# Performance work log

Measured on AMD Instinct MI355X. Metric: run time of the kernel, lower is better.

Reference implementation:

```python
import jax, jax.numpy as jnp
import numpy as np

B, N = 2, 2048
TOP_K = 48
NUM_RBF = 16
MAX_REL = 32            # max_relative_feature
NUM_POS = 16            # num_positional_embeddings
EDGE_FEATURES = 128
EDGE_IN = NUM_POS + NUM_RBF * 25  # 416
POS_IN = 2 * MAX_REL + 2          # 66 one-hot classes


def setup_inputs() -> dict:
    key = jax.random.key(0)
    k0, k1, k2, k3 = jax.random.split(key, 4)
    X = jax.random.normal(k0, (B, N, 4, 3), dtype=jnp.float32) * 3.0
    mask = jnp.ones((B, N), dtype=jnp.float32)
    R_idx = jnp.arange(B * N, dtype=jnp.int32).reshape(B, N)
    chain_labels = jax.random.randint(k1, (B, N), 0, 4).astype(jnp.int32)
    W_pos = 0.05 * jax.random.normal(k2, (POS_IN, NUM_POS), dtype=jnp.float32)
    b_pos = jnp.zeros((NUM_POS,), dtype=jnp.float32)
    W_edge = 0.05 * jax.random.normal(k3, (EDGE_IN, EDGE_FEATURES), dtype=jnp.float32)
    b_edge = jnp.zeros((EDGE_FEATURES,), dtype=jnp.float32)
    return {"X": X, "mask": mask, "R_idx": R_idx, "chain_labels": chain_labels,
            "W_pos": W_pos, "b_pos": b_pos, "W_edge": W_edge, "b_edge": b_edge}


def _rbf(D):
    # D: [..., K] -> [..., K, NUM_RBF]
    mu = jnp.linspace(2.0, 22.0, NUM_RBF)        # D_min=2, D_max=22
    sigma = (22.0 - 2.0) / NUM_RBF               # 1.25
    return jnp.exp(-(((D[..., None] - mu) / sigma) ** 2))


def _pair_dist(A, Bc):
    # A, Bc: [B, N, 3] -> [B, N, N]
    return jnp.sqrt(jnp.sum((A[:, :, None, :] - Bc[:, None, :, :]) ** 2, axis=-1) + 1e-6)


def reference(X, mask, R_idx, chain_labels, W_pos, b_pos, W_edge, b_edge):
    # virtual Cbeta from backbone geometry
    b = X[:, :, 1, :] - X[:, :, 0, :]
    c = X[:, :, 2, :] - X[:, :, 1, :]
    a = jnp.cross(b, c, axis=-1)
    Cb = -0.58273431 * a + 0.56802827 * b - 0.54067466 * c + X[:, :, 1, :]
    Ca, Nat, Cat, Oat = X[:, :, 1, :], X[:, :, 0, :], X[:, :, 2, :], X[:, :, 3, :]

    # masked Ca-Ca distances + k nearest neighbors
    mask2 = mask[:, None, :] * mask[:, :, None]
    D = mask2 * _pair_dist(Ca, Ca)
    D_adjust = D + (1.0 - mask2) * jnp.max(D, axis=-1, keepdims=True)
    neg_D, E_idx = jax.lax.top_k(-D_adjust, min(TOP_K, N))  # smallest distances
    D_neighbors = -neg_D                                     # [B, N, K]

    rbfs = [_rbf(D_neighbors)]
    pairs = [(Nat, Nat), (Cat, Cat), (Oat, Oat), (Cb, Cb),
             (Ca, Nat), (Ca, Cat), (Ca, Oat), (Ca, Cb),
             (Nat, Cat), (Nat, Oat), (Nat, Cb), (Cb, Cat), (Cb, Oat), (Oat, Cat),
             (Nat, Ca), (Cat, Ca), (Oat, Ca), (Cb, Ca),
             (Cat, Nat), (Oat, Nat), (Cb, Nat), (Cat, Cb), (Oat, Cb), (Cat, Oat)]
    for A_, B_ in pairs:  # fixed structural set of 24 atom-pair types
        Dab = _pair_dist(A_, B_)                          # [B, N, N]
        Dn = jnp.take_along_axis(Dab, E_idx, axis=2)      # [B, N, K]
        rbfs.append(_rbf(Dn))
    RBF_all = jnp.concatenate(rbfs, axis=-1)              # [B, N, K, 25*NUM_RBF]

    # relative positional / chain features at the gathered neighbors
    offset = R_idx[:, :, None] - R_idx[:, None, :]
    offset = jnp.take_along_axis(offset, E_idx, axis=2)   # [B, N, K]
    d_chains = (chain_labels[:, :, None] == chain_labels[:, None, :]).astype(jnp.int32)
    E_chains = jnp.take_along_axis(d_chains, E_idx, axis=2)

    d = jnp.clip(offset + MAX_REL, 0, 2 * MAX_REL)
    d = d * E_chains + (1 - E_chains) * (2 * MAX_REL + 1)
    d_onehot = jax.nn.one_hot(d, POS_IN, dtype=jnp.float32)  # [B, N, K, 66]
    E_positional = d_onehot @ W_pos + b_pos                  # [B, N, K, 16]

    E = jnp.concatenate((E_positional, RBF_all), axis=-1)    # [B, N, K, 416]
    E = E @ W_edge + b_edge                                  # [B, N, K, 128]
    return E, E_idx
```

## Files before the change

### kernel.cpp

```cpp
#include <hip/hip_runtime.h>
#include <hip/hip_bf16.h>
#include <stdint.h>

#define BB   2
#define NN   2048
#define BN   (BB*NN)
#define KTOP 48
#define EIN  416
#define EF   128

typedef __attribute__((ext_vector_type(8))) short s8v;
typedef __attribute__((ext_vector_type(4))) float f32x4;
typedef __attribute__((ext_vector_type(4))) unsigned int u32x4;
typedef unsigned short u16;
typedef unsigned int u32;
typedef unsigned long long u64;

__device__ __constant__ int cPA[25] = {1,0,2,3,4,1,1,1,1,0,0,0,4,4,3,0,2,3,4,2,3,4,2,3,2};
__device__ __constant__ int cPB[25] = {1,0,2,3,4,0,2,3,4,2,3,4,2,3,2,1,1,1,1,0,0,0,4,4,3};

__device__ __forceinline__ u16 bf16u(float x) {
  __hip_bfloat16 h = __float2bfloat16(x);
  return *reinterpret_cast<u16*>(&h);
}
__device__ __forceinline__ u32 cvtpk(float lo, float hi) {
  u32 r;
  asm("v_cvt_pk_bf16_f32 %0, %1, %2" : "=v"(r) : "v"(lo), "v"(hi));
  return r;
}

__global__ __launch_bounds__(256) void prep_kernel(const float* __restrict__ X,
                                                   const float* __restrict__ W_edge,
                                                   float* __restrict__ atoms5p,
                                                   float* __restrict__ capack4,
                                                   u16* __restrict__ wtf) {
  int tid = blockIdx.x * 256 + threadIdx.x;
  if (tid < EIN * EF) {
    int k = tid >> 7, n = tid & 127;
    wtf[((size_t)(k >> 3)) * 1024 + n * 8 + (k & 7)] = bf16u(W_edge[tid]);
  } else if (tid < EIN * EF + BN) {
    int idx = tid - EIN * EF;
    const float* x = X + (size_t)idx * 12;
    float Nx = x[0], Ny = x[1], Nz = x[2];
    float Cax = x[3], Cay = x[4], Caz = x[5];
    float Cx = x[6], Cy = x[7], Cz = x[8];
    float Ox = x[9], Oy = x[10], Oz = x[11];
    float bx = Cax - Nx, by = Cay - Ny, bz = Caz - Nz;
    float cx = Cx - Cax, cy = Cy - Cay, cz = Cz - Caz;
    float ax = by * cz - bz * cy;
    float ay = bz * cx - bx * cz;
    float az = bx * cy - by * cx;
    float Cbx = -0.58273431f * ax + 0.56802827f * bx - 0.54067466f * cx + Cax;
    float Cby = -0.58273431f * ay + 0.56802827f * by - 0.54067466f * cy + Cay;
    float Cbz = -0.58273431f * az + 0.56802827f * bz - 0.54067466f * cz + Caz;
    f32x4* o = (f32x4*)(atoms5p + (size_t)idx * 20);
    o[0] = (f32x4){Nx, Ny, Nz, 0.f};
    o[1] = (f32x4){Cax, Cay, Caz, 0.f};
    o[2] = (f32x4){Cx, Cy, Cz, 0.f};
    o[3] = (f32x4){Ox, Oy, Oz, 0.f};
    o[4] = (f32x4){Cbx, Cby, Cbz, 0.f};
    *(f32x4*)(capack4 + (size_t)idx * 4) = (f32x4){Cax, Cay, Caz, 0.f};
  }
}

__device__ __forceinline__ u32 blockExclScan(u32 v, u32* scanw, int t) {
  int lane = t & 63, w = t >> 6;
  u32 inc = v;
#pragma unroll
  for (int off = 1; off < 64; off <<= 1) {
    u32 o = __shfl_up(inc, off);
    if (lane >= off) inc += o;
  }
  if (lane == 63) scanw[w] = inc;
  __syncthreads();
  u32 base = 0;
  for (int ww = 0; ww < w; ++ww) base += scanw[ww];
  __syncthreads();
  return base + inc - v;
}

template<int NB, bool CHKPREF>
__device__ __forceinline__ void radix_round(u32* hist, u32* scanw, u32* selinfo, int t,
                                            const u32* kv, u32 pref, int prefShift,
                                            int binShift, u32 binMask, u32 r) {
  const int PB = NB / 256;
#pragma unroll
  for (int q = 0; q < PB / 4; ++q)
    *(u32x4*)&hist[t * PB + q * 4] = (u32x4){0, 0, 0, 0};
  __syncthreads();
#pragma unroll
  for (int s = 0; s < 8; ++s) {
    bool ok = (!CHKPREF) || ((kv[s] >> prefShift) == pref);
    if (ok) atomicAdd(&hist[(kv[s] >> binShift) & binMask], 1u);
  }
  __syncthreads();
  u32 loc[PB];
  u32 sum = 0;
#pragma unroll
  for (int q = 0; q < PB / 4; ++q) {
    u32x4 lv = *(u32x4*)&hist[t * PB + q * 4];
    loc[q * 4 + 0] = lv.x; loc[q * 4 + 1] = lv.y;
    loc[q * 4 + 2] = lv.z; loc[q * 4 + 3] = lv.w;
    sum += lv.x + lv.y + lv.z + lv.w;
  }
  int lane = t & 63, w = t >> 6;
  u32 inc = sum;
#pragma unroll
  for (int off = 1; off < 64; off <<= 1) {
    u32 o = __shfl_up(inc, off);
    if (lane >= off) inc += o;
  }
  if (lane == 63) scanw[w] = inc;
  __syncthreads();
  u32 base = 0;
  for (int ww = 0; ww < w; ++ww) base += scanw[ww];
  u32 c = base + inc - sum;
#pragma unroll
  for (int q = 0; q < PB; ++q) {
    u32 nc = c + loc[q];
    if (c < r && r <= nc) { selinfo[0] = (u32)(t * PB + q); selinfo[1] = r - c; }
    c = nc;
  }
  __syncthreads();
}

__global__ __launch_bounds__(256) void topk_kernel(const float* __restrict__ capack4,
                                                   const float* __restrict__ mask,
                                                   float* __restrict__ dtop,
                                                   float* __restrict__ eidx_f) {
  __shared__ u32 hist[4096];
  __shared__ u32 scanw[4];
  __shared__ u32 selinfo[2];
  __shared__ float redf[4];
  __shared__ u64 win[64];

  int row = blockIdx.x;
  int b = row >> 11, i = row & (NN - 1);
  int t = threadIdx.x, lane = t & 63, w = t >> 6;
  const float* cab4 = capack4 + (size_t)b * NN * 4;
  const float* mrow = mask + (size_t)b * NN;
  f32x4 ci = *(const f32x4*)&cab4[(size_t)i * 4];
  float mi = mrow[i];
  f32x4 mk0 = *(const f32x4*)&mrow[t * 8];
  f32x4 mk1 = *(const f32x4*)&mrow[t * 8 + 4];

  float dvv[8], m2v[8];
  float lmax = 0.f;
#pragma unroll
  for (int s = 0; s < 8; ++s) {
    f32x4 cj = *(const f32x4*)&cab4[(size_t)(t * 8 + s) * 4];
    float dx = ci.x - cj.x, dy = ci.y - cj.y, dz = ci.z - cj.z;
    float d = sqrtf(dx * dx + dy * dy + dz * dz + 1e-6f);
    float mj = (s < 4) ? mk0[s] : mk1[s - 4];
    float m2 = mi * mj;
    float D = m2 * d;
    dvv[s] = D; m2v[s] = m2;
    lmax = fmaxf(lmax, D);
  }
#pragma unroll
  for (int off = 32; off >= 1; off >>= 1) lmax = fmaxf(lmax, __shfl_xor(lmax, off));
  if (lane == 0) redf[w] = lmax;
  __syncthreads();
  float rmax = fmaxf(fmaxf(redf[0], redf[1]), fmaxf(redf[2], redf[3]));

  u32 kv[8];
#pragma unroll
  for (int s = 0; s < 8; ++s)
    kv[s] = __float_as_uint(dvv[s] + (1.0f - m2v[s]) * rmax);

  u32 r = KTOP;
  radix_round<4096, false>(hist, scanw, selinfo, t, kv, 0, 0, 20, 0xFFFu, r);
  u32 sel1 = selinfo[0]; r = selinfo[1];
  radix_round<1024, true>(hist, scanw, selinfo, t, kv, sel1, 20, 10, 0x3FFu, r);
  u32 sel2 = selinfo[0]; r = selinfo[1];
  u32 pref12 = (sel1 << 10) | sel2;
  radix_round<1024, true>(hist, scanw, selinfo, t, kv, pref12, 10, 0, 0x3FFu, r);
  u32 sel3 = selinfo[0];
  u32 takeEq = selinfo[1];
  u32 T = (sel1 << 20) | (sel2 << 10) | sel3;

  u32 lcnt = 0, ecnt = 0;
#pragma unroll
  for (int s = 0; s < 8; ++s) { lcnt += (kv[s] < T); ecnt += (kv[s] == T); }
  u32 ebase = blockExclScan(ecnt, scanw, t);
  u32 taken = 0;
  if (ebase < takeEq) { u32 room = takeEq - ebase; taken = room < ecnt ? room : ecnt; }
  u32 wbase = blockExclScan(lcnt + taken, scanw, t);
  u32 slot = wbase, tleft = taken;
#pragma unroll
  for (int s = 0; s < 8; ++s) {
    u32 j = (u32)(t * 8 + s);
    if (kv[s] < T) {
      win[slot++] = ((u64)kv[s] << 32) | j;
    } else if (kv[s] == T && tleft) {
      win[slot++] = ((u64)kv[s] << 32) | j;
      tleft--;
    }
  }
  __syncthreads();

  if (w == 0) {
    u64 key = (lane < KTOP) ? win[lane] : ~0ull;
#pragma unroll
    for (int k = 2; k <= 64; k <<= 1) {
#pragma unroll
      for (int jj = k >> 1; jj >= 1; jj >>= 1) {
        u64 p = __shfl_xor(key, jj);
        bool lowerl = (lane & jj) == 0;
        bool asc = (lane & k) == 0;
        u64 mn = p < key ? p : key;
        u64 mx = p < key ? key : p;
        key = (lowerl == asc) ? mn : mx;
      }
    }
    if (lane < KTOP) {
      u32 j = (u32)(key & 0xffffffffu);
      eidx_f[row * KTOP + lane] = (float)j;
      dtop[row * KTOP + lane] = __uint_as_float((u32)(key >> 32));
    }
  }
}

__device__ __forceinline__ s8v rbf8(float D, float mu0) {
  float Dc = fminf(D, 40.0f);
  float t0 = (Dc - mu0) * 0.8f;
  float v0 = __expf(-t0 * t0);
  float g = __expf(fmaf(2.13333333f, t0, -1.13777778f));
  const float C = 0.10273985f;
  float v1 = v0 * g; g *= C;
  float v2 = v1 * g; g *= C;
  float v3 = v2 * g; g *= C;
  float v4 = v3 * g; g *= C;
  float v5 = v4 * g; g *= C;
  float v6 = v5 * g; g *= C;
  float v7 = v6 * g;
  union { u32x4 u; s8v s; } cv;
  cv.u = (u32x4){cvtpk(v0, v1), cvtpk(v2, v3), cvtpk(v4, v5), cvtpk(v6, v7)};
  return cv.s;
}

#define STAGE(bufi, kcs) do {                                                        \
  const u16* _s = wtf + (kcs) * 4096 + t * 8;                                        \
  __builtin_amdgcn_global_load_lds(                                                  \
      (const __attribute__((address_space(1))) u32*)_s,                              \
      (__attribute__((address_space(3))) u32*)&bbuf[bufi][t * 8], 16, 0, 0);         \
  __builtin_amdgcn_global_load_lds(                                                  \
      (const __attribute__((address_space(1))) u32*)(_s + 2048),                     \
      (__attribute__((address_space(3))) u32*)&bbuf[bufi][t * 8 + 2048], 16, 0, 0);  \
} while (0)

__global__ __launch_bounds__(256, 4) void edge_kernel(const float* __restrict__ atoms5p,
                                                      const u16* __restrict__ wtf,
                                                      const float* __restrict__ eidx_f,
                                                      const float* __restrict__ dtop,
                                                      const int* __restrict__ Ridx,
                                                      const int* __restrict__ chains,
                                                      const float* __restrict__ Wpos,
                                                      const float* __restrict__ bpos,
                                                      const float* __restrict__ bedge,
                                                      float* __restrict__ Eout) {
  __shared__ __align__(16) u16 bbuf[2][4096];

  static constexpr int kPA[25] = {1,0,2,3,4,1,1,1,1,0,0,0,4,4,3,0,2,3,4,2,3,4,2,3,2};
  static constexpr int kPB[25] = {1,0,2,3,4,0,2,3,4,2,3,4,2,3,2,1,1,1,1,0,0,0,4,4,3};

  int t = threadIdx.x;
  int lane = t & 63, w = t >> 6;
  int lr = lane & 15, lg = lane >> 4;

  int task = blockIdx.x * 4 + w;
  int row = task / 3, mt = task - row * 3;
  int b = row >> 11, i = row & (NN - 1);
  int kbase = mt * 16;
  const float* atomsB = atoms5p + (size_t)b * NN * 20;

  int kk = kbase + lr;
  int j = (int)eidx_f[(size_t)row * KTOP + kk];
  float dtv = dtop[(size_t)row * KTOP + kk];

  f32x4 I[5], J[5];
#pragma unroll
  for (int a = 0; a < 5; ++a) {
    I[a] = *(const f32x4*)&atomsB[(size_t)i * 20 + a * 4];
    J[a] = *(const f32x4*)&atomsB[(size_t)j * 20 + a * 4];
  }

  bool hi = (lg >= 2);
  float D[12];
#pragma unroll
  for (int q = 0; q < 12; ++q) {
    int pO = 2 * q + 1, pE = 2 * q + 2;
    f32x4 Iv = hi ? I[kPA[pE]] : I[kPA[pO]];
    f32x4 Jv = hi ? J[kPB[pE]] : J[kPB[pO]];
    float dx = Iv.x - Jv.x, dy = Iv.y - Jv.y, dz = Iv.z - Jv.z;
    D[q] = __builtin_amdgcn_sqrtf(dx * dx + dy * dy + dz * dz + 1e-6f);
  }

  const float MU8 = 12.6666667f;
  s8v af0;
  if (lg < 2) {
    int Ri = Ridx[b * NN + i], Rj = Ridx[b * NN + j];
    int same = (chains[b * NN + i] == chains[b * NN + j]);
    int off = Ri - Rj + 32;
    off = off < 0 ? 0 : (off > 64 ? 64 : off);
    int drow = same ? off : 65;
    const float* wr = Wpos + drow * 16 + lg * 8;
    f32x4 w0 = *(const f32x4*)wr;
    f32x4 w1 = *(const f32x4*)(wr + 4);
    f32x4 b0 = *(const f32x4*)(bpos + lg * 8);
    f32x4 b1 = *(const f32x4*)(bpos + lg * 8 + 4);
    union { u32x4 u; s8v s; } cv;
    cv.u = (u32x4){cvtpk(w0.x + b0.x, w0.y + b0.y), cvtpk(w0.z + b0.z, w0.w + b0.w),
                   cvtpk(w1.x + b1.x, w1.y + b1.y), cvtpk(w1.z + b1.z, w1.w + b1.w)};
    af0 = cv.s;
  } else {
    af0 = rbf8(dtv, (lg == 2) ? 2.0f : MU8);
  }

  f32x4 acc[8] = {};
  STAGE(0, 0);
  __syncthreads();
#pragma unroll
  for (int kc = 0; kc < 13; ++kc) {
    if (kc < 12) STAGE((kc + 1) & 1, kc + 1);
    s8v af = (kc == 0) ? af0 : rbf8(D[kc - 1], (lg & 1) ? MU8 : 2.0f);
    const u16* bb = &bbuf[kc & 1][lg * 1024 + lr * 8];
#pragma unroll
    for (int nt = 0; nt < 8; ++nt) {
      s8v bv = *(const s8v*)(bb + nt * 128);
      acc[nt] = __builtin_amdgcn_mfma_f32_16x16x32_bf16(af, bv, acc[nt], 0, 0, 0);
    }
    __syncthreads();
  }

  float bias[8];
#pragma unroll
  for (int nt = 0; nt < 8; ++nt) bias[nt] = bedge[nt * 16 + lr];
  float* orow = Eout + ((size_t)row * KTOP + kbase) * EF;
#pragma unroll
  for (int qq = 0; qq < 4; ++qq) {
    float* pr = orow + (size_t)(lg * 4 + qq) * EF + lr;
#pragma unroll
    for (int nt = 0; nt < 8; ++nt)
      pr[nt * 16] = acc[nt][qq] + bias[nt];
  }
}

extern "C" void kernel_launch(void* const* d_in, const int* in_sizes, int n_in,
                              void* d_out, int out_size, void* d_ws, size_t ws_size,
                              hipStream_t stream) {
  const float* X = (const float*)d_in[0];
  const float* mask = (const float*)d_in[1];
  const int* Ridx = (const int*)d_in[2];
  const int* chains = (const int*)d_in[3];
  const float* Wpos = (const float*)d_in[4];
  const float* bpos = (const float*)d_in[5];
  const float* Wedge = (const float*)d_in[6];
  const float* bedge = (const float*)d_in[7];

  float* Eout = (float*)d_out;
  float* EidxF = Eout + (size_t)BN * KTOP * EF;

  u16* wtf = (u16*)d_ws;
  float* atoms5p = (float*)((char*)d_ws + 53248 * 2);
  float* capack4 = atoms5p + (size_t)BN * 20;
  float* dtop = capack4 + (size_t)BN * 4;

  prep_kernel<<<(EIN * EF + BN + 255) / 256, 256, 0, stream>>>(X, Wedge, atoms5p, capack4, wtf);
  topk_kernel<<<BN, 256, 0, stream>>>(capack4, mask, dtop, EidxF);
  edge_kernel<<<BN * 3 / 4, 256, 0, stream>>>(atoms5p, wtf, EidxF, dtop, Ridx, chains, Wpos, bpos, bedge, Eout);
}
```

Measured before the change: 115.4 us.

## Process full 48-neighbor row per wave and stage weights in two large chunks

Each wave now handles all three 16-neighbor tiles of a row, so every B-fragment read from LDS feeds three MFMAs instead of one. The weight matrix is loaded into LDS in two big batches (7 then 6 k-chunks), replacing the per-chunk double buffer with its barrier after every step. This raises registers per thread (three accumulator sets, 36 distances) and shared memory to 56KB, so occupancy drops (launch bounds go from 4 to 2). The grid shrinks to a third, which may leave fewer waves available to hide latency.

```diff
diff --git a/kernel.cpp b/kernel.cpp
--- a/kernel.cpp
+++ b/kernel.cpp
@@ -239,17 +239,7 @@
   return cv.s;
 }
 
-#define STAGE(bufi, kcs) do {                                                        \
-  const u16* _s = wtf + (kcs) * 4096 + t * 8;                                        \
-  __builtin_amdgcn_global_load_lds(                                                  \
-      (const __attribute__((address_space(1))) u32*)_s,                              \
-      (__attribute__((address_space(3))) u32*)&bbuf[bufi][t * 8], 16, 0, 0);         \
-  __builtin_amdgcn_global_load_lds(                                                  \
-      (const __attribute__((address_space(1))) u32*)(_s + 2048),                     \
-      (__attribute__((address_space(3))) u32*)&bbuf[bufi][t * 8 + 2048], 16, 0, 0);  \
-} while (0)
-
-__global__ __launch_bounds__(256, 4) void edge_kernel(const float* __restrict__ atoms5p,
+__global__ __launch_bounds__(256, 2) void edge_kernel(const float* __restrict__ atoms5p,
                                                       const u16* __restrict__ wtf,
                                                       const float* __restrict__ eidx_f,
                                                       const float* __restrict__ dtop,
@@ -259,7 +249,7 @@
                                                       const float* __restrict__ bpos,
                                                       const float* __restrict__ bedge,
                                                       float* __restrict__ Eout) {
-  __shared__ __align__(16) u16 bbuf[2][4096];
+  __shared__ __align__(16) u16 bbuf[7 * 4096];
 
   static constexpr int kPA[25] = {1,0,2,3,4,1,1,1,1,0,0,0,4,4,3,0,2,3,4,2,3,4,2,3,2};
   static constexpr int kPB[25] = {1,0,2,3,4,0,2,3,4,2,3,4,2,3,2,1,1,1,1,0,0,0,4,4,3};
@@ -267,82 +257,127 @@
   int t = threadIdx.x;
   int lane = t & 63, w = t >> 6;
   int lr = lane & 15, lg = lane >> 4;
-
-  int task = blockIdx.x * 4 + w;
-  int row = task / 3, mt = task - row * 3;
+  bool hi = (lg >= 2);
+
+  int row = blockIdx.x * 4 + w;
   int b = row >> 11, i = row & (NN - 1);
-  int kbase = mt * 16;
   const float* atomsB = atoms5p + (size_t)b * NN * 20;
 
-  int kk = kbase + lr;
-  int j = (int)eidx_f[(size_t)row * KTOP + kk];
-  float dtv = dtop[(size_t)row * KTOP + kk];
-
-  f32x4 I[5], J[5];
-#pragma unroll
-  for (int a = 0; a < 5; ++a) {
+#pragma unroll
+  for (int r2 = 0; r2 < 14; ++r2) {
+    const u16* src = wtf + r2 * 2048 + t * 8;
+    __builtin_amdgcn_global_load_lds(
+        (const __attribute__((address_space(1))) u32*)src,
+        (__attribute__((address_space(3))) u32*)&bbuf[r2 * 2048 + t * 8], 16, 0, 0);
+  }
+
+  f32x4 I[5];
+#pragma unroll
+  for (int a = 0; a < 5; ++a)
     I[a] = *(const f32x4*)&atomsB[(size_t)i * 20 + a * 4];
-    J[a] = *(const f32x4*)&atomsB[(size_t)j * 20 + a * 4];
-  }
-
-  bool hi = (lg >= 2);
-  float D[12];
-#pragma unroll
-  for (int q = 0; q < 12; ++q) {
-    int pO = 2 * q + 1, pE = 2 * q + 2;
-    f32x4 Iv = hi ? I[kPA[pE]] : I[kPA[pO]];
-    f32x4 Jv = hi ? J[kPB[pE]] : J[kPB[pO]];
-    float dx = Iv.x - Jv.x, dy = Iv.y - Jv.y, dz = Iv.z - Jv.z;
-    D[q] = __builtin_amdgcn_sqrtf(dx * dx + dy * dy + dz * dz + 1e-6f);
-  }
+  int Ri = Ridx[b * NN + i];
+  int chi = chains[b * NN + i];
 
   const float MU8 = 12.6666667f;
-  s8v af0;
-  if (lg < 2) {
-    int Ri = Ridx[b * NN + i], Rj = Ridx[b * NN + j];
-    int same = (chains[b * NN + i] == chains[b * NN + j]);
-    int off = Ri - Rj + 32;
-    off = off < 0 ? 0 : (off > 64 ? 64 : off);
-    int drow = same ? off : 65;
-    const float* wr = Wpos + drow * 16 + lg * 8;
-    f32x4 w0 = *(const f32x4*)wr;
-    f32x4 w1 = *(const f32x4*)(wr + 4);
-    f32x4 b0 = *(const f32x4*)(bpos + lg * 8);
-    f32x4 b1 = *(const f32x4*)(bpos + lg * 8 + 4);
-    union { u32x4 u; s8v s; } cv;
-    cv.u = (u32x4){cvtpk(w0.x + b0.x, w0.y + b0.y), cvtpk(w0.z + b0.z, w0.w + b0.w),
-                   cvtpk(w1.x + b1.x, w1.y + b1.y), cvtpk(w1.z + b1.z, w1.w + b1.w)};
-    af0 = cv.s;
-  } else {
-    af0 = rbf8(dtv, (lg == 2) ? 2.0f : MU8);
-  }
-
-  f32x4 acc[8] = {};
-  STAGE(0, 0);
-  __syncthreads();
-#pragma unroll
-  for (int kc = 0; kc < 13; ++kc) {
-    if (kc < 12) STAGE((kc + 1) & 1, kc + 1);
-    s8v af = (kc == 0) ? af0 : rbf8(D[kc - 1], (lg & 1) ? MU8 : 2.0f);
-    const u16* bb = &bbuf[kc & 1][lg * 1024 + lr * 8];
+  float D[3][12];
+  s8v af0[3];
+#pragma unroll
+  for (int mt = 0; mt < 3; ++mt) {
+    int kk = mt * 16 + lr;
+    int j = (int)eidx_f[(size_t)row * KTOP + kk];
+    float dtv = dtop[(size_t)row * KTOP + kk];
+    f32x4 J[5];
+#pragma unroll
+    for (int a = 0; a < 5; ++a)
+      J[a] = *(const f32x4*)&atomsB[(size_t)j * 20 + a * 4];
+#pragma unroll
+    for (int q = 0; q < 12; ++q) {
+      f32x4 Iv = hi ? I[kPA[2 * q + 2]] : I[kPA[2 * q + 1]];
+      f32x4 Jv = hi ? J[kPB[2 * q + 2]] : J[kPB[2 * q + 1]];
+      float dx = Iv.x - Jv.x, dy = Iv.y - Jv.y, dz = Iv.z - Jv.z;
+      D[mt][q] = __builtin_amdgcn_sqrtf(dx * dx + dy * dy + dz * dz + 1e-6f);
+    }
+    if (lg < 2) {
+      int Rj = Ridx[b * NN + j];
+      int same = (chi == chains[b * NN + j]);
+      int off = Ri - Rj + 32;
+      off = off < 0 ? 0 : (off > 64 ? 64 : off);
+      int drow = same ? off : 65;
+      const float* wr = Wpos + drow * 16 + lg * 8;
+      f32x4 w0 = *(const f32x4*)wr;
+      f32x4 w1 = *(const f32x4*)(wr + 4);
+      f32x4 b0 = *(const f32x4*)(bpos + lg * 8);
+      f32x4 b1 = *(const f32x4*)(bpos + lg * 8 + 4);
+      union { u32x4 u; s8v s; } cv;
+      cv.u = (u32x4){cvtpk(w0.x + b0.x, w0.y + b0.y), cvtpk(w0.z + b0.z, w0.w + b0.w),
+                     cvtpk(w1.x + b1.x, w1.y + b1.y), cvtpk(w1.z + b1.z, w1.w + b1.w)};
+      af0[mt] = cv.s;
+    } else {
+      af0[mt] = rbf8(dtv, (lg == 2) ? 2.0f : MU8);
+    }
+  }
+  float mu0 = (lg & 1) ? MU8 : 2.0f;
+
+  __syncthreads();
+
+  f32x4 acc0[8] = {}, acc1[8] = {}, acc2[8] = {};
+
+#pragma unroll
+  for (int kc = 0; kc < 7; ++kc) {
+    s8v a0 = kc ? rbf8(D[0][kc - 1], mu0) : af0[0];
+    s8v a1 = kc ? rbf8(D[1][kc - 1], mu0) : af0[1];
+    s8v a2 = kc ? rbf8(D[2][kc - 1], mu0) : af0[2];
+    const u16* bb = &bbuf[kc * 4096 + lg * 1024 + lr * 8];
 #pragma unroll
     for (int nt = 0; nt < 8; ++nt) {
       s8v bv = *(const s8v*)(bb + nt * 128);
-      acc[nt] = __builtin_amdgcn_mfma_f32_16x16x32_bf16(af, bv, acc[nt], 0, 0, 0);
-    }
-    __syncthreads();
+      acc0[nt] = __builtin_amdgcn_mfma_f32_16x16x32_bf16(a0, bv, acc0[nt], 0, 0, 0);
+      acc1[nt] = __builtin_amdgcn_mfma_f32_16x16x32_bf16(a1, bv, acc1[nt], 0, 0, 0);
+      acc2[nt] = __builtin_amdgcn_mfma_f32_16x16x32_bf16(a2, bv, acc2[nt], 0, 0, 0);
+    }
+  }
+
+  __syncthreads();
+
+#pragma unroll
+  for (int r2 = 0; r2 < 12; ++r2) {
+    const u16* src = wtf + 7 * 4096 + r2 * 2048 + t * 8;
+    __builtin_amdgcn_global_load_lds(
+        (const __attribute__((address_space(1))) u32*)src,
+        (__attribute__((address_space(3))) u32*)&bbuf[r2 * 2048 + t * 8], 16, 0, 0);
+  }
+  __syncthreads();
+
+#pragma unroll
+  for (int kc = 7; kc < 13; ++kc) {
+    s8v a0 = rbf8(D[0][kc - 1], mu0);
+    s8v a1 = rbf8(D[1][kc - 1], mu0);
+    s8v a2 = rbf8(D[2][kc - 1], mu0);
+    const u16* bb = &bbuf[(kc - 7) * 4096 + lg * 1024 + lr * 8];
+#pragma unroll
+    for (int nt = 0; nt < 8; ++nt) {
+      s8v bv = *(const s8v*)(bb + nt * 128);
+      acc0[nt] = __builtin_amdgcn_mfma_f32_16x16x32_bf16(a0, bv, acc0[nt], 0, 0, 0);
+      acc1[nt] = __builtin_amdgcn_mfma_f32_16x16x32_bf16(a1, bv, acc1[nt], 0, 0, 0);
+      acc2[nt] = __builtin_amdgcn_mfma_f32_16x16x32_bf16(a2, bv, acc2[nt], 0, 0, 0);
+    }
   }
 
   float bias[8];
 #pragma unroll
   for (int nt = 0; nt < 8; ++nt) bias[nt] = bedge[nt * 16 + lr];
-  float* orow = Eout + ((size_t)row * KTOP + kbase) * EF;
+  float* orow = Eout + (size_t)row * KTOP * EF;
 #pragma unroll
   for (int qq = 0; qq < 4; ++qq) {
-    float* pr = orow + (size_t)(lg * 4 + qq) * EF + lr;
-#pragma unroll
-    for (int nt = 0; nt < 8; ++nt)
-      pr[nt * 16] = acc[nt][qq] + bias[nt];
+    float* p0 = orow + (size_t)(lg * 4 + qq) * EF + lr;
+    float* p1 = orow + (size_t)(16 + lg * 4 + qq) * EF + lr;
+    float* p2 = orow + (size_t)(32 + lg * 4 + qq) * EF + lr;
+#pragma unroll
+    for (int nt = 0; nt < 8; ++nt) {
+      p0[nt * 16] = acc0[nt][qq] + bias[nt];
+      p1[nt * 16] = acc1[nt][qq] + bias[nt];
+      p2[nt * 16] = acc2[nt][qq] + bias[nt];
+    }
   }
 }
 
@@ -368,5 +403,5 @@
 
   prep_kernel<<<(EIN * EF + BN + 255) / 256, 256, 0, stream>>>(X, Wedge, atoms5p, capack4, wtf);
   topk_kernel<<<BN, 256, 0, stream>>>(capack4, mask, dtop, EidxF);
-  edge_kernel<<<BN * 3 / 4, 256, 0, stream>>>(atoms5p, wtf, EidxF, dtop, Ridx, chains, Wpos, bpos, bedge, Eout);
-}
+  edge_kernel<<<BN / 4, 256, 0, stream>>>(atoms5p, wtf, EidxF, dtop, Ridx, chains, Wpos, bpos, bedge, Eout);
+}
```

Measured after the change: 427.0 us. 3.7x slower.

## Use 1024-thread blocks with weights resident in LDS, one row per wave

Applied to the files above, without the earlier changes.

The edge kernel now launches 1024-thread blocks. Each block stages the first 8 K-chunks of the bf16 edge weight matrix into 64KB of LDS once, and each wave loops over all 3 neighbor tiles of one row. The remaining 5 chunks are read straight from global memory (through cache). This removes the per-chunk double-buffered staging and the per-iteration __syncthreads, and it reuses the i-atom loads across tiles. The cost is 64KB of LDS per block, which limits occupancy, and global-latency loads inside the MFMA loop for the tail chunks.

```diff
diff --git a/kernel.cpp b/kernel.cpp
--- a/kernel.cpp
+++ b/kernel.cpp
@@ -239,27 +239,17 @@
   return cv.s;
 }
 
-#define STAGE(bufi, kcs) do {                                                        \
-  const u16* _s = wtf + (kcs) * 4096 + t * 8;                                        \
-  __builtin_amdgcn_global_load_lds(                                                  \
-      (const __attribute__((address_space(1))) u32*)_s,                              \
-      (__attribute__((address_space(3))) u32*)&bbuf[bufi][t * 8], 16, 0, 0);         \
-  __builtin_amdgcn_global_load_lds(                                                  \
-      (const __attribute__((address_space(1))) u32*)(_s + 2048),                     \
-      (__attribute__((address_space(3))) u32*)&bbuf[bufi][t * 8 + 2048], 16, 0, 0);  \
-} while (0)
-
-__global__ __launch_bounds__(256, 4) void edge_kernel(const float* __restrict__ atoms5p,
-                                                      const u16* __restrict__ wtf,
-                                                      const float* __restrict__ eidx_f,
-                                                      const float* __restrict__ dtop,
-                                                      const int* __restrict__ Ridx,
-                                                      const int* __restrict__ chains,
-                                                      const float* __restrict__ Wpos,
-                                                      const float* __restrict__ bpos,
-                                                      const float* __restrict__ bedge,
-                                                      float* __restrict__ Eout) {
-  __shared__ __align__(16) u16 bbuf[2][4096];
+__global__ __launch_bounds__(1024, 4) void edge_kernel(const float* __restrict__ atoms5p,
+                                                       const u16* __restrict__ wtf,
+                                                       const float* __restrict__ eidx_f,
+                                                       const float* __restrict__ dtop,
+                                                       const int* __restrict__ Ridx,
+                                                       const int* __restrict__ chains,
+                                                       const float* __restrict__ Wpos,
+                                                       const float* __restrict__ bpos,
+                                                       const float* __restrict__ bedge,
+                                                       float* __restrict__ Eout) {
+  __shared__ __align__(16) u16 bbuf[8 * 4096];
 
   static constexpr int kPA[25] = {1,0,2,3,4,1,1,1,1,0,0,0,4,4,3,0,2,3,4,2,3,4,2,3,2};
   static constexpr int kPB[25] = {1,0,2,3,4,0,2,3,4,2,3,4,2,3,2,1,1,1,1,0,0,0,4,4,3};
@@ -267,82 +257,106 @@
   int t = threadIdx.x;
   int lane = t & 63, w = t >> 6;
   int lr = lane & 15, lg = lane >> 4;
-
-  int task = blockIdx.x * 4 + w;
-  int row = task / 3, mt = task - row * 3;
+  bool hi = (lg >= 2);
+
+#pragma unroll
+  for (int it = 0; it < 4; ++it) {
+    const u16* src = wtf + it * 8192 + t * 8;
+    __builtin_amdgcn_global_load_lds(
+        (const __attribute__((address_space(1))) u32*)src,
+        (__attribute__((address_space(3))) u32*)&bbuf[it * 8192 + t * 8], 16, 0, 0);
+  }
+
+  int row = blockIdx.x * 16 + w;
   int b = row >> 11, i = row & (NN - 1);
-  int kbase = mt * 16;
   const float* atomsB = atoms5p + (size_t)b * NN * 20;
 
-  int kk = kbase + lr;
-  int j = (int)eidx_f[(size_t)row * KTOP + kk];
-  float dtv = dtop[(size_t)row * KTOP + kk];
-
-  f32x4 I[5], J[5];
-#pragma unroll
-  for (int a = 0; a < 5; ++a) {
+  f32x4 I[5];
+#pragma unroll
+  for (int a = 0; a < 5; ++a)
     I[a] = *(const f32x4*)&atomsB[(size_t)i * 20 + a * 4];
-    J[a] = *(const f32x4*)&atomsB[(size_t)j * 20 + a * 4];
-  }
-
-  bool hi = (lg >= 2);
-  float D[12];
-#pragma unroll
-  for (int q = 0; q < 12; ++q) {
-    int pO = 2 * q + 1, pE = 2 * q + 2;
-    f32x4 Iv = hi ? I[kPA[pE]] : I[kPA[pO]];
-    f32x4 Jv = hi ? J[kPB[pE]] : J[kPB[pO]];
-    float dx = Iv.x - Jv.x, dy = Iv.y - Jv.y, dz = Iv.z - Jv.z;
-    D[q] = __builtin_amdgcn_sqrtf(dx * dx + dy * dy + dz * dz + 1e-6f);
-  }
+  int Ri = Ridx[b * NN + i];
+  int chi = chains[b * NN + i];
+  float bias[8];
+#pragma unroll
+  for (int nt = 0; nt < 8; ++nt) bias[nt] = bedge[nt * 16 + lr];
 
   const float MU8 = 12.6666667f;
-  s8v af0;
-  if (lg < 2) {
-    int Ri = Ridx[b * NN + i], Rj = Ridx[b * NN + j];
-    int same = (chains[b * NN + i] == chains[b * NN + j]);
-    int off = Ri - Rj + 32;
-    off = off < 0 ? 0 : (off > 64 ? 64 : off);
-    int drow = same ? off : 65;
-    const float* wr = Wpos + drow * 16 + lg * 8;
-    f32x4 w0 = *(const f32x4*)wr;
-    f32x4 w1 = *(const f32x4*)(wr + 4);
-    f32x4 b0 = *(const f32x4*)(bpos + lg * 8);
-    f32x4 b1 = *(const f32x4*)(bpos + lg * 8 + 4);
-    union { u32x4 u; s8v s; } cv;
-    cv.u = (u32x4){cvtpk(w0.x + b0.x, w0.y + b0.y), cvtpk(w0.z + b0.z, w0.w + b0.w),
-                   cvtpk(w1.x + b1.x, w1.y + b1.y), cvtpk(w1.z + b1.z, w1.w + b1.w)};
-    af0 = cv.s;
-  } else {
-    af0 = rbf8(dtv, (lg == 2) ? 2.0f : MU8);
-  }
-
-  f32x4 acc[8] = {};
-  STAGE(0, 0);
-  __syncthreads();
-#pragma unroll
-  for (int kc = 0; kc < 13; ++kc) {
-    if (kc < 12) STAGE((kc + 1) & 1, kc + 1);
-    s8v af = (kc == 0) ? af0 : rbf8(D[kc - 1], (lg & 1) ? MU8 : 2.0f);
-    const u16* bb = &bbuf[kc & 1][lg * 1024 + lr * 8];
-#pragma unroll
-    for (int nt = 0; nt < 8; ++nt) {
-      s8v bv = *(const s8v*)(bb + nt * 128);
-      acc[nt] = __builtin_amdgcn_mfma_f32_16x16x32_bf16(af, bv, acc[nt], 0, 0, 0);
-    }
-    __syncthreads();
-  }
-
-  float bias[8];
-#pragma unroll
-  for (int nt = 0; nt < 8; ++nt) bias[nt] = bedge[nt * 16 + lr];
-  float* orow = Eout + ((size_t)row * KTOP + kbase) * EF;
-#pragma unroll
-  for (int qq = 0; qq < 4; ++qq) {
-    float* pr = orow + (size_t)(lg * 4 + qq) * EF + lr;
-#pragma unroll
-    for (int nt = 0; nt < 8; ++nt)
-      pr[nt * 16] = acc[nt][qq] + bias[nt];
+  float mu0 = (lg & 1) ? MU8 : 2.0f;
+
+  __syncthreads();
+
+  for (int mt = 0; mt < 3; ++mt) {
+    int kk = mt * 16 + lr;
+    int j = (int)eidx_f[(size_t)row * KTOP + kk];
+    float dtv = dtop[(size_t)row * KTOP + kk];
+
+    float D[12];
+    {
+      f32x4 J[5];
+#pragma unroll
+      for (int a = 0; a < 5; ++a)
+        J[a] = *(const f32x4*)&atomsB[(size_t)j * 20 + a * 4];
+#pragma unroll
+      for (int q = 0; q < 12; ++q) {
+        f32x4 Iv = hi ? I[kPA[2 * q + 2]] : I[kPA[2 * q + 1]];
+        f32x4 Jv = hi ? J[kPB[2 * q + 2]] : J[kPB[2 * q + 1]];
+        float dx = Iv.x - Jv.x, dy = Iv.y - Jv.y, dz = Iv.z - Jv.z;
+        D[q] = __builtin_amdgcn_sqrtf(dx * dx + dy * dy + dz * dz + 1e-6f);
+      }
+    }
+
+    s8v af0;
+    if (lg < 2) {
+      int Rj = Ridx[b * NN + j];
+      int same = (chi == chains[b * NN + j]);
+      int off = Ri - Rj + 32;
+      off = off < 0 ? 0 : (off > 64 ? 64 : off);
+      int drow = same ? off : 65;
+      const float* wr = Wpos + drow * 16 + lg * 8;
+      f32x4 w0 = *(const f32x4*)wr;
+      f32x4 w1 = *(const f32x4*)(wr + 4);
+      f32x4 b0 = *(const f32x4*)(bpos + lg * 8);
+      f32x4 b1 = *(const f32x4*)(bpos + lg * 8 + 4);
+      union { u32x4 u; s8v s; } cv;
+      cv.u = (u32x4){cvtpk(w0.x + b0.x, w0.y + b0.y), cvtpk(w0.z + b0.z, w0.w + b0.w),
+                     cvtpk(w1.x + b1.x, w1.y + b1.y), cvtpk(w1.z + b1.z, w1.w + b1.w)};
+      af0 = cv.s;
+    } else {
+      af0 = rbf8(dtv, (lg == 2) ? 2.0f : MU8);
+    }
+
+    f32x4 acc[8] = {};
+
+#pragma unroll
+    for (int kc = 0; kc < 8; ++kc) {
+      s8v af = kc ? rbf8(D[kc - 1], mu0) : af0;
+      const u16* bb = &bbuf[kc * 4096 + lg * 1024 + lr * 8];
+#pragma unroll
+      for (int nt = 0; nt < 8; ++nt) {
+        s8v bv = *(const s8v*)(bb + nt * 128);
+        acc[nt] = __builtin_amdgcn_mfma_f32_16x16x32_bf16(af, bv, acc[nt], 0, 0, 0);
+      }
+    }
+#pragma unroll
+    for (int kc = 8; kc < 13; ++kc) {
+      s8v af = rbf8(D[kc - 1], mu0);
+      const u16* bg = wtf + (size_t)kc * 4096 + lg * 1024 + lr * 8;
+#pragma unroll
+      for (int nt = 0; nt < 8; ++nt) {
+        s8v bv = *(const s8v*)(bg + nt * 128);
+        acc[nt] = __builtin_amdgcn_mfma_f32_16x16x32_bf16(af, bv, acc[nt], 0, 0, 0);
+      }
+    }
+
+    float* orow = Eout + ((size_t)row * KTOP + mt * 16) * EF;
+#pragma unroll
+    for (int qq = 0; qq < 4; ++qq) {
+      float* pr = orow + (size_t)(lg * 4 + qq) * EF + lr;
+#pragma unroll
+      for (int nt = 0; nt < 8; ++nt)
+        pr[nt * 16] = acc[nt][qq] + bias[nt];
+    }
   }
 }
 
@@ -368,5 +382,5 @@
 
   prep_kernel<<<(EIN * EF + BN + 255) / 256, 256, 0, stream>>>(X, Wedge, atoms5p, capack4, wtf);
   topk_kernel<<<BN, 256, 0, stream>>>(capack4, mask, dtop, EidxF);
-  edge_kernel<<<BN * 3 / 4, 256, 0, stream>>>(atoms5p, wtf, EidxF, dtop, Ridx, chains, Wpos, bpos, bedge, Eout);
-}
+  edge_kernel<<<BN / 16, 1024, 0, stream>>>(atoms5p, wtf, EidxF, dtop, Ridx, chains, Wpos, bpos, bedge, Eout);
+}
```

After: 188.1 us. +62.9%, slower.
